# Optimization experiments

Hardware: AMD Instinct MI355X
Metric: run time of the kernel (lower is better)

Reference implementation:

```python
import jax, jax.numpy as jnp
import numpy as np

B, N, F, H, MH = 8, 1024, 768, 12, 3072
DH = F // H
EPS = 1e-5

def _ln(x, g, b):
    mu = jnp.mean(x, axis=-1, keepdims=True)
    var = jnp.mean(jnp.square(x - mu), axis=-1, keepdims=True)
    return (x - mu) * jax.lax.rsqrt(var + EPS) * g + b

def setup_inputs() -> dict:
    key = jax.random.key(0)
    ks = jax.random.split(key, 16)
    s = 1.0 / np.sqrt(F)
    sm = 1.0 / np.sqrt(MH)
    return {
        "x": jax.random.normal(ks[0], (B, N, F), dtype=jnp.float32),
        "Wq": jax.random.uniform(ks[1], (F, F), jnp.float32, -s, s),
        "bq": jax.random.uniform(ks[2], (F,), jnp.float32, -s, s),
        "Wk": jax.random.uniform(ks[3], (F, F), jnp.float32, -s, s),
        "bk": jax.random.uniform(ks[4], (F,), jnp.float32, -s, s),
        "Wv": jax.random.uniform(ks[5], (F, F), jnp.float32, -s, s),
        "bv": jax.random.uniform(ks[6], (F,), jnp.float32, -s, s),
        "Wo": jax.random.uniform(ks[7], (F, F), jnp.float32, -s, s),
        "bo": jax.random.uniform(ks[8], (F,), jnp.float32, -s, s),
        "ln1_g": jnp.ones((F,), jnp.float32),
        "ln1_b": jnp.zeros((F,), jnp.float32),
        "ln2_g": jnp.ones((F,), jnp.float32),
        "ln2_b": jnp.zeros((F,), jnp.float32),
        "W1": jax.random.uniform(ks[9], (F, MH), jnp.float32, -s, s),
        "b1": jax.random.uniform(ks[10], (MH,), jnp.float32, -s, s),
        "W2": jax.random.uniform(ks[11], (MH, F), jnp.float32, -sm, sm),
        "b2": jax.random.uniform(ks[12], (F,), jnp.float32, -sm, sm),
    }

def reference(x, Wq, bq, Wk, bk, Wv, bv, Wo, bo, ln1_g, ln1_b, ln2_g, ln2_b, W1, b1, W2, b2):
    xn = _ln(x, ln1_g, ln1_b)
    # low-rank (here full-rank, rank=-1) QKV projections, split into heads -> [b,h,n,dh]
    q = (xn @ Wq + bq).reshape(B, N, H, DH).transpose(0, 2, 1, 3)
    k = (xn @ Wk + bk).reshape(B, N, H, DH).transpose(0, 2, 1, 3)
    v = (xn @ Wv + bv).reshape(B, N, H, DH).transpose(0, 2, 1, 3)
    # note: original scales by sqrt(feats), NOT sqrt(d_head)
    score = jax.nn.softmax(jnp.einsum('bhif,bhjf->bhij', q, k) / jnp.sqrt(jnp.float32(F)), axis=-1)
    attn = jnp.einsum('bhij,bhjf->bhif', score, v)
    attn = attn.transpose(0, 2, 1, 3).reshape(B, N, F)
    out = (attn @ Wo + bo) + x  # dropout p=0.0
    h = _ln(out, ln2_g, ln2_b)
    h = jax.nn.gelu(h @ W1 + b1, approximate=False)
    h = jax.nn.gelu(h @ W2 + b2, approximate=False)  # second GELU per source
    return h + out
```

## Files before the change

kernel.cpp:

```cpp
#include <hip/hip_runtime.h>
#include <math.h>

#define B_ 8
#define N_ 1024
#define F_ 768
#define H_ 12
#define DH_ 64
#define MH_ 3072
#define MROWS (B_ * N_)

typedef unsigned short u16;
typedef unsigned int u32;
typedef __bf16 bf16x8 __attribute__((ext_vector_type(8)));
typedef float f32x4 __attribute__((ext_vector_type(4)));

__device__ inline f32x4 mfma16(bf16x8 a, bf16x8 b, f32x4 c) {
  return __builtin_amdgcn_mfma_f32_16x16x32_bf16(a, b, c, 0, 0, 0);
}

__device__ inline u16 f2bu(float f) {
  u32 b = __builtin_bit_cast(u32, f);
  b += 0x7fffu + ((b >> 16) & 1u);
  return (u16)(b >> 16);
}
__device__ inline float bu2f(u16 u) {
  u32 x = ((u32)u) << 16;
  return __builtin_bit_cast(float, x);
}
__device__ inline float gelu_exact(float x) {
  return 0.5f * x * (1.0f + erff(x * 0.70710678118654752f));
}

#define AS1 __attribute__((address_space(1)))
#define AS3 __attribute__((address_space(3)))
__device__ inline void glds16(const void* g, void* l) {
  __builtin_amdgcn_global_load_lds((const AS1 void*)g, (AS3 void*)l, 16, 0, 0);
}

__device__ inline float ldf(const float* p) { return *p; }
__device__ inline float ldf(const u16* p) { return bu2f(*p); }

template <typename Tin>
__global__ __launch_bounds__(256) void transpose_bf16(
    const Tin* __restrict__ in, u16* __restrict__ out, int R, int C) {
  __shared__ float tile[64][65];
  size_t ibase = (size_t)blockIdx.z * (size_t)R * (size_t)C;
  size_t obase = (size_t)blockIdx.z * (size_t)R * (size_t)C;
  int r0 = blockIdx.y << 6, c0 = blockIdx.x << 6;
  int t = threadIdx.x;
#pragma unroll
  for (int i = 0; i < 16; ++i) {
    int idx = t + (i << 8);
    int r = idx >> 6, c = idx & 63;
    tile[r][c] = ldf(&in[ibase + (size_t)(r0 + r) * C + (c0 + c)]);
  }
  __syncthreads();
#pragma unroll
  for (int i = 0; i < 16; ++i) {
    int idx = t + (i << 8);
    int rr = idx >> 6, cc = idx & 63;
    out[obase + (size_t)(c0 + rr) * R + (r0 + cc)] = f2bu(tile[cc][rr]);
  }
}

__global__ __launch_bounds__(256) void concat_bias(
    const float* __restrict__ a, const float* __restrict__ b,
    const float* __restrict__ c, float* __restrict__ o) {
  int i = blockIdx.x * 256 + threadIdx.x;
  if (i < 768) o[i] = a[i];
  else if (i < 1536) o[i] = b[i - 768];
  else o[i] = c[i - 1536];
}

__global__ __launch_bounds__(256) void ln_to_bf16(
    const float* __restrict__ X, const float* __restrict__ gw,
    const float* __restrict__ bw, u16* __restrict__ Y) {
  int row = blockIdx.x;
  int t = threadIdx.x;
  const float* xr = X + (size_t)row * F_;
  float v0 = xr[t], v1 = xr[t + 256], v2 = xr[t + 512];
  float s = v0 + v1 + v2;
  float ss = v0 * v0 + v1 * v1 + v2 * v2;
#pragma unroll
  for (int off = 1; off < 64; off <<= 1) {
    s += __shfl_xor(s, off, 64);
    ss += __shfl_xor(ss, off, 64);
  }
  __shared__ float red[8];
  int wid = t >> 6, lane = t & 63;
  if (lane == 0) { red[wid] = s; red[4 + wid] = ss; }
  __syncthreads();
  s = red[0] + red[1] + red[2] + red[3];
  ss = red[4] + red[5] + red[6] + red[7];
  float mu = s * (1.0f / F_);
  float var = ss * (1.0f / F_) - mu * mu;
  float rstd = rsqrtf(var + 1e-5f);
  u16* yr = Y + (size_t)row * F_;
  yr[t] = f2bu((v0 - mu) * rstd * gw[t] + bw[t]);
  yr[t + 256] = f2bu((v1 - mu) * rstd * gw[t + 256] + bw[t + 256]);
  yr[t + 512] = f2bu((v2 - mu) * rstd * gw[t + 512] + bw[t + 512]);
}

template <int MODE>
__global__ __launch_bounds__(256) void gemm_bt(
    const u16* __restrict__ A, const u16* __restrict__ Bt,
    const float* __restrict__ bias, void* __restrict__ outp,
    const float* __restrict__ resid, int Ndim, int Kdim, float qscale) {
  __shared__ __attribute__((aligned(16))) u16 As[2][128][32];
  __shared__ __attribute__((aligned(16))) u16 Bs[2][128][32];
  int t = threadIdx.x;
  int lane = t & 63, wid = t >> 6;

  int nwg = gridDim.x;
  int q8 = nwg >> 3;
  int bid = blockIdx.x;
  int swz = (bid & 7) * q8 + (bid >> 3);
  int nnt = Ndim >> 7;
  int mt = swz / nnt, nt = swz - mt * nnt;
  int row0 = mt << 7, col0 = nt << 7;

  int wr = (wid >> 1) << 6, wc = (wid & 1) << 6;
  int lr = lane & 15, lk = (lane >> 4) << 3;
  int rbase = (lane >> 4) << 2;
  f32x4 zero = {0.f, 0.f, 0.f, 0.f};
  f32x4 acc[4][4];
#pragma unroll
  for (int m = 0; m < 4; ++m)
#pragma unroll
    for (int n = 0; n < 4; ++n) acc[m][n] = zero;

  int o0 = (wid << 10) + (lane << 4);
  int srow = o0 >> 6;
  int scol = (o0 & 63) >> 1;
  const u16* Ag = A + (size_t)(row0 + srow) * Kdim + scol;
  const u16* Bg = Bt + (size_t)(col0 + srow) * Kdim + scol;
  char* AsB = (char*)&As[0][0][0] + (wid << 10);
  char* BsB = (char*)&Bs[0][0][0] + (wid << 10);
  size_t half = (size_t)64 * Kdim;

  auto STAGE = [&](int buf, int kt) {
    int bo = buf << 13;
    glds16(Ag + kt, AsB + bo);
    glds16(Ag + kt + half, AsB + bo + 4096);
    glds16(Bg + kt, BsB + bo);
    glds16(Bg + kt + half, BsB + bo + 4096);
  };

  STAGE(0, 0);
  __syncthreads();
  int nk = Kdim >> 5;
  for (int ki = 0; ki < nk; ++ki) {
    int buf = ki & 1;
    if (ki + 1 < nk) STAGE(buf ^ 1, (ki + 1) << 5);
    bf16x8 af[4], bfr[4];
#pragma unroll
    for (int m = 0; m < 4; ++m) af[m] = *(const bf16x8*)&As[buf][wr + (m << 4) + lr][lk];
#pragma unroll
    for (int n = 0; n < 4; ++n) bfr[n] = *(const bf16x8*)&Bs[buf][wc + (n << 4) + lr][lk];
#pragma unroll
    for (int m = 0; m < 4; ++m)
#pragma unroll
      for (int n = 0; n < 4; ++n) acc[m][n] = mfma16(af[m], bfr[n], acc[m][n]);
    __syncthreads();
  }

#pragma unroll
  for (int n = 0; n < 4; ++n) {
    int col = col0 + wc + (n << 4) + lr;
    float bc = bias[col];
    int sub = 0, hh = 0, dh = 0;
    float sc = 1.0f;
    if constexpr (MODE == 0) {
      sub = (col >= 1536) ? 2 : (col >= 768 ? 1 : 0);
      int c = col - sub * 768;
      hh = c >> 6; dh = c & 63;
      sc = (sub == 0) ? qscale : 1.0f;
    }
#pragma unroll
    for (int m = 0; m < 4; ++m) {
#pragma unroll
      for (int r = 0; r < 4; ++r) {
        int row = row0 + wr + (m << 4) + rbase + r;
        float val = acc[m][n][r] + bc;
        if constexpr (MODE == 0) {
          int b = row >> 10, nn = row & 1023;
          ((u16*)outp)[(size_t)sub * 6291456 +
                       ((((size_t)b * H_ + hh) << 10) + nn) * DH_ + dh] = f2bu(val * sc);
        } else if constexpr (MODE == 1) {
          val += resid[(size_t)row * Ndim + col];
          ((float*)outp)[(size_t)row * Ndim + col] = val;
        } else if constexpr (MODE == 2) {
          ((u16*)outp)[(size_t)row * Ndim + col] = f2bu(gelu_exact(val));
        } else {
          val = gelu_exact(val) + resid[(size_t)row * Ndim + col];
          ((float*)outp)[(size_t)row * Ndim + col] = val;
        }
      }
    }
  }
}

__global__ __launch_bounds__(256, 3) void attn_fwd(
    const u16* __restrict__ Q, const u16* __restrict__ K,
    const u16* __restrict__ Vt, u16* __restrict__ Aout) {
  __shared__ __attribute__((aligned(16))) u16 Ks[64][72];
  __shared__ __attribute__((aligned(16))) u16 Vs[64][72];
  __shared__ __attribute__((aligned(16))) u16 Ps[4][32][72];
  int t = threadIdx.x, lane = t & 63, wid = t >> 6;

  int bid = blockIdx.x;
  int swz = (bid & 7) * 96 + (bid >> 3);
  int bh = swz >> 3;
  int qt = swz & 7;
  int q0 = (qt << 7) + (wid << 5);

  int lr = lane & 15, lk = (lane >> 4) << 3;
  int rbase = (lane >> 4) << 2;

  bf16x8 qf[2][2];
#pragma unroll
  for (int m = 0; m < 2; ++m)
#pragma unroll
    for (int ks = 0; ks < 2; ++ks)
      qf[m][ks] = *(const bf16x8*)&Q[((size_t)bh * N_ + q0 + (m << 4) + lr) * DH_ + (ks << 5) + lk];

  float lsum[2][4];
  f32x4 zero = {0.f, 0.f, 0.f, 0.f};
  f32x4 Oacc[2][4];
#pragma unroll
  for (int m = 0; m < 2; ++m) {
#pragma unroll
    for (int r = 0; r < 4; ++r) lsum[m][r] = 0.f;
#pragma unroll
    for (int nd = 0; nd < 4; ++nd) Oacc[m][nd] = zero;
  }

  int srow = t >> 3;
  int scol = (t & 7) << 3;
  const u16* Kg = K + ((size_t)bh * N_ + srow) * DH_ + scol;
  const u16* Vg = Vt + ((size_t)bh * DH_ + srow) * N_ + scol;

  for (int kt = 0; kt < 16; ++kt) {
    __syncthreads();
    *(uint4*)&Ks[srow][scol]      = *(const uint4*)(Kg + (size_t)(kt << 6) * DH_);
    *(uint4*)&Ks[srow + 32][scol] = *(const uint4*)(Kg + (size_t)((kt << 6) + 32) * DH_);
    *(uint4*)&Vs[srow][scol]      = *(const uint4*)(Vg + (kt << 6));
    *(uint4*)&Vs[srow + 32][scol] = *(const uint4*)(Vg + (size_t)32 * N_ + (kt << 6));
    __syncthreads();

    f32x4 s[2][4];
#pragma unroll
    for (int m = 0; m < 2; ++m)
#pragma unroll
      for (int n = 0; n < 4; ++n) s[m][n] = zero;
#pragma unroll
    for (int ks = 0; ks < 2; ++ks) {
      bf16x8 kf[4];
#pragma unroll
      for (int n = 0; n < 4; ++n) kf[n] = *(const bf16x8*)&Ks[(n << 4) + lr][(ks << 5) + lk];
#pragma unroll
      for (int m = 0; m < 2; ++m)
#pragma unroll
        for (int n = 0; n < 4; ++n) s[m][n] = mfma16(qf[m][ks], kf[n], s[m][n]);
    }

#pragma unroll
    for (int m = 0; m < 2; ++m)
#pragma unroll
      for (int n = 0; n < 4; ++n)
#pragma unroll
        for (int r = 0; r < 4; ++r) {
          float p = exp2f(s[m][n][r]);
          lsum[m][r] += p;
          Ps[wid][(m << 4) + rbase + r][(n << 4) + lr] = f2bu(p);
        }

#pragma unroll
    for (int ks = 0; ks < 2; ++ks) {
      bf16x8 pf[2], vf[4];
#pragma unroll
      for (int m = 0; m < 2; ++m) pf[m] = *(const bf16x8*)&Ps[wid][(m << 4) + lr][(ks << 5) + lk];
#pragma unroll
      for (int nd = 0; nd < 4; ++nd) vf[nd] = *(const bf16x8*)&Vs[(nd << 4) + lr][(ks << 5) + lk];
#pragma unroll
      for (int m = 0; m < 2; ++m)
#pragma unroll
        for (int nd = 0; nd < 4; ++nd) Oacc[m][nd] = mfma16(pf[m], vf[nd], Oacc[m][nd]);
    }
  }

  int b = bh / H_, h = bh % H_;
#pragma unroll
  for (int m = 0; m < 2; ++m)
#pragma unroll
    for (int r = 0; r < 4; ++r) {
      float sv = lsum[m][r];
#pragma unroll
      for (int off = 1; off < 16; off <<= 1) sv += __shfl_xor(sv, off, 64);
      float inv = 1.0f / sv;
      int row = q0 + (m << 4) + rbase + r;
      size_t orow = ((size_t)b * N_ + row) * F_ + (size_t)h * DH_;
#pragma unroll
      for (int nd = 0; nd < 4; ++nd)
        Aout[orow + (nd << 4) + lr] = f2bu(Oacc[m][nd][r] * inv);
    }
}

extern "C" void kernel_launch(void* const* d_in, const int* in_sizes, int n_in,
                              void* d_out, int out_size, void* d_ws, size_t ws_size,
                              hipStream_t stream) {
  (void)in_sizes; (void)n_in; (void)out_size; (void)ws_size;
  const float* x   = (const float*)d_in[0];
  const float* Wq  = (const float*)d_in[1];
  const float* bq  = (const float*)d_in[2];
  const float* Wk  = (const float*)d_in[3];
  const float* bk  = (const float*)d_in[4];
  const float* Wv  = (const float*)d_in[5];
  const float* bv  = (const float*)d_in[6];
  const float* Wo  = (const float*)d_in[7];
  const float* bo  = (const float*)d_in[8];
  const float* g1  = (const float*)d_in[9];
  const float* bn1 = (const float*)d_in[10];
  const float* g2  = (const float*)d_in[11];
  const float* bn2 = (const float*)d_in[12];
  const float* W1  = (const float*)d_in[13];
  const float* b1  = (const float*)d_in[14];
  const float* W2  = (const float*)d_in[15];
  const float* b2  = (const float*)d_in[16];

  char* ws = (char*)d_ws;
  size_t off = 0;
  auto alloc = [&](size_t bytes) {
    char* p = ws + off;
    off += (bytes + 255) & ~(size_t)255;
    return p;
  };
  u16* Wqkvt = (u16*)alloc((size_t)3 * F_ * F_ * 2);
  u16* Wot  = (u16*)alloc((size_t)F_ * F_ * 2);
  u16* W1t  = (u16*)alloc((size_t)MH_ * F_ * 2);
  u16* W2t  = (u16*)alloc((size_t)MH_ * F_ * 2);
  float* bqkv = (float*)alloc((size_t)3 * F_ * 4);
  u16* xn  = (u16*)alloc((size_t)MROWS * F_ * 2);
  u16* qb  = (u16*)alloc((size_t)B_ * H_ * N_ * DH_ * 2);
  u16* kb  = (u16*)alloc((size_t)B_ * H_ * N_ * DH_ * 2);
  u16* vb  = (u16*)alloc((size_t)B_ * H_ * N_ * DH_ * 2);
  u16* vt  = (u16*)alloc((size_t)B_ * H_ * N_ * DH_ * 2);
  u16* attn = (u16*)alloc((size_t)MROWS * F_ * 2);
  float* outb = (float*)alloc((size_t)MROWS * F_ * 4);
  u16* h1 = qb;
  u16* hn = xn;

  const float QSCALE = 0.052058773227f;

  dim3 blk(256);
  transpose_bf16<float><<<dim3(12, 12, 1), blk, 0, stream>>>(Wq, Wqkvt, F_, F_);
  transpose_bf16<float><<<dim3(12, 12, 1), blk, 0, stream>>>(Wk, Wqkvt + (size_t)F_ * F_, F_, F_);
  transpose_bf16<float><<<dim3(12, 12, 1), blk, 0, stream>>>(Wv, Wqkvt + (size_t)2 * F_ * F_, F_, F_);
  transpose_bf16<float><<<dim3(12, 12, 1), blk, 0, stream>>>(Wo, Wot, F_, F_);
  transpose_bf16<float><<<dim3(48, 12, 1), blk, 0, stream>>>(W1, W1t, F_, MH_);
  transpose_bf16<float><<<dim3(12, 48, 1), blk, 0, stream>>>(W2, W2t, MH_, F_);
  concat_bias<<<dim3(9), blk, 0, stream>>>(bq, bk, bv, bqkv);
  ln_to_bf16<<<dim3(MROWS), blk, 0, stream>>>(x, g1, bn1, xn);
  gemm_bt<0><<<dim3(18 * 64), blk, 0, stream>>>(xn, Wqkvt, bqkv, qb, nullptr, 3 * F_, F_, QSCALE);
  transpose_bf16<u16><<<dim3(1, 16, 96), blk, 0, stream>>>(vb, vt, N_, DH_);
  attn_fwd<<<dim3(768), blk, 0, stream>>>(qb, kb, vt, attn);
  gemm_bt<1><<<dim3(6 * 64), blk, 0, stream>>>(attn, Wot, bo, outb, x, F_, F_, 1.0f);
  ln_to_bf16<<<dim3(MROWS), blk, 0, stream>>>(outb, g2, bn2, hn);
  gemm_bt<2><<<dim3(24 * 64), blk, 0, stream>>>(hn, W1t, b1, h1, nullptr, MH_, F_, 1.0f);
  gemm_bt<3><<<dim3(6 * 64), blk, 0, stream>>>(h1, W2t, b2, d_out, outb, F_, MH_, 1.0f);
}
```

Baseline: 318.7 us.

## Shrink GEMM tiles to 128x64, merge weight prep kernels, prefetch attention KV

```diff
diff --git a/kernel.cpp b/kernel.cpp
--- a/kernel.cpp
+++ b/kernel.cpp
@@ -37,39 +37,58 @@
   __builtin_amdgcn_global_load_lds((const AS1 void*)g, (AS3 void*)l, 16, 0, 0);
 }
 
-__device__ inline float ldf(const float* p) { return *p; }
-__device__ inline float ldf(const u16* p) { return bu2f(*p); }
-
-template <typename Tin>
-__global__ __launch_bounds__(256) void transpose_bf16(
-    const Tin* __restrict__ in, u16* __restrict__ out, int R, int C) {
+__global__ __launch_bounds__(256) void prep_weights(
+    const float* __restrict__ Wq, const float* __restrict__ Wk,
+    const float* __restrict__ Wv, const float* __restrict__ Wo,
+    const float* __restrict__ W1, const float* __restrict__ W2,
+    u16* __restrict__ Wqkvt, u16* __restrict__ Wot,
+    u16* __restrict__ W1t, u16* __restrict__ W2t) {
   __shared__ float tile[64][65];
-  size_t ibase = (size_t)blockIdx.z * (size_t)R * (size_t)C;
-  size_t obase = (size_t)blockIdx.z * (size_t)R * (size_t)C;
+  int z = blockIdx.z;
+  const float* in; u16* out; int R, C;
+  if (z == 0)      { in = Wq; out = Wqkvt;                       R = 768;  C = 768; }
+  else if (z == 1) { in = Wk; out = Wqkvt + 768 * 768;           R = 768;  C = 768; }
+  else if (z == 2) { in = Wv; out = Wqkvt + 2 * 768 * 768;       R = 768;  C = 768; }
+  else if (z == 3) { in = Wo; out = Wot;                         R = 768;  C = 768; }
+  else if (z == 4) { in = W1; out = W1t;                         R = 768;  C = 3072; }
+  else             { in = W2; out = W2t;                         R = 3072; C = 768; }
   int r0 = blockIdx.y << 6, c0 = blockIdx.x << 6;
+  if (r0 >= R || c0 >= C) return;
   int t = threadIdx.x;
 #pragma unroll
   for (int i = 0; i < 16; ++i) {
     int idx = t + (i << 8);
     int r = idx >> 6, c = idx & 63;
-    tile[r][c] = ldf(&in[ibase + (size_t)(r0 + r) * C + (c0 + c)]);
+    tile[r][c] = in[(size_t)(r0 + r) * C + (c0 + c)];
   }
   __syncthreads();
 #pragma unroll
   for (int i = 0; i < 16; ++i) {
     int idx = t + (i << 8);
     int rr = idx >> 6, cc = idx & 63;
-    out[obase + (size_t)(c0 + rr) * R + (r0 + cc)] = f2bu(tile[cc][rr]);
-  }
-}
-
-__global__ __launch_bounds__(256) void concat_bias(
-    const float* __restrict__ a, const float* __restrict__ b,
-    const float* __restrict__ c, float* __restrict__ o) {
-  int i = blockIdx.x * 256 + threadIdx.x;
-  if (i < 768) o[i] = a[i];
-  else if (i < 1536) o[i] = b[i - 768];
-  else o[i] = c[i - 1536];
+    out[(size_t)(c0 + rr) * R + (r0 + cc)] = f2bu(tile[cc][rr]);
+  }
+}
+
+__global__ __launch_bounds__(256) void transpose_v(
+    const u16* __restrict__ in, u16* __restrict__ out, int R, int C) {
+  __shared__ float tile[64][65];
+  size_t base = (size_t)blockIdx.z * (size_t)R * (size_t)C;
+  int r0 = blockIdx.y << 6, c0 = blockIdx.x << 6;
+  int t = threadIdx.x;
+#pragma unroll
+  for (int i = 0; i < 16; ++i) {
+    int idx = t + (i << 8);
+    int r = idx >> 6, c = idx & 63;
+    tile[r][c] = bu2f(in[base + (size_t)(r0 + r) * C + (c0 + c)]);
+  }
+  __syncthreads();
+#pragma unroll
+  for (int i = 0; i < 16; ++i) {
+    int idx = t + (i << 8);
+    int rr = idx >> 6, cc = idx & 63;
+    out[base + (size_t)(c0 + rr) * R + (r0 + cc)] = f2bu(tile[cc][rr]);
+  }
 }
 
 __global__ __launch_bounds__(256) void ln_to_bf16(
@@ -102,12 +121,13 @@
 }
 
 template <int MODE>
-__global__ __launch_bounds__(256) void gemm_bt(
+__global__ __launch_bounds__(256, 4) void gemm_t(
     const u16* __restrict__ A, const u16* __restrict__ Bt,
-    const float* __restrict__ bias, void* __restrict__ outp,
+    const float* __restrict__ b0, const float* __restrict__ b1,
+    const float* __restrict__ b2, void* __restrict__ outp,
     const float* __restrict__ resid, int Ndim, int Kdim, float qscale) {
   __shared__ __attribute__((aligned(16))) u16 As[2][128][32];
-  __shared__ __attribute__((aligned(16))) u16 Bs[2][128][32];
+  __shared__ __attribute__((aligned(16))) u16 Bs[2][64][32];
   int t = threadIdx.x;
   int lane = t & 63, wid = t >> 6;
 
@@ -115,23 +135,23 @@
   int q8 = nwg >> 3;
   int bid = blockIdx.x;
   int swz = (bid & 7) * q8 + (bid >> 3);
-  int nnt = Ndim >> 7;
+  int nnt = Ndim >> 6;
   int mt = swz / nnt, nt = swz - mt * nnt;
-  int row0 = mt << 7, col0 = nt << 7;
-
-  int wr = (wid >> 1) << 6, wc = (wid & 1) << 6;
+  int row0 = mt << 7, col0 = nt << 6;
+
+  int wr = (wid >> 1) << 6;
+  int wc = (wid & 1) << 5;
   int lr = lane & 15, lk = (lane >> 4) << 3;
   int rbase = (lane >> 4) << 2;
   f32x4 zero = {0.f, 0.f, 0.f, 0.f};
-  f32x4 acc[4][4];
+  f32x4 acc[4][2];
 #pragma unroll
   for (int m = 0; m < 4; ++m)
 #pragma unroll
-    for (int n = 0; n < 4; ++n) acc[m][n] = zero;
-
-  int o0 = (wid << 10) + (lane << 4);
-  int srow = o0 >> 6;
-  int scol = (o0 & 63) >> 1;
+    for (int n = 0; n < 2; ++n) acc[m][n] = zero;
+
+  int srow = (wid << 4) + (lane >> 2);
+  int scol = (lane & 3) << 3;
   const u16* Ag = A + (size_t)(row0 + srow) * Kdim + scol;
   const u16* Bg = Bt + (size_t)(col0 + srow) * Kdim + scol;
   char* AsB = (char*)&As[0][0][0] + (wid << 10);
@@ -139,11 +159,9 @@
   size_t half = (size_t)64 * Kdim;
 
   auto STAGE = [&](int buf, int kt) {
-    int bo = buf << 13;
-    glds16(Ag + kt, AsB + bo);
-    glds16(Ag + kt + half, AsB + bo + 4096);
-    glds16(Bg + kt, BsB + bo);
-    glds16(Bg + kt + half, BsB + bo + 4096);
+    glds16(Ag + kt, AsB + (buf << 13));
+    glds16(Ag + kt + half, AsB + (buf << 13) + 4096);
+    glds16(Bg + kt, BsB + (buf << 12));
   };
 
   STAGE(0, 0);
@@ -152,29 +170,32 @@
   for (int ki = 0; ki < nk; ++ki) {
     int buf = ki & 1;
     if (ki + 1 < nk) STAGE(buf ^ 1, (ki + 1) << 5);
-    bf16x8 af[4], bfr[4];
+    bf16x8 af[4], bfr[2];
 #pragma unroll
     for (int m = 0; m < 4; ++m) af[m] = *(const bf16x8*)&As[buf][wr + (m << 4) + lr][lk];
 #pragma unroll
-    for (int n = 0; n < 4; ++n) bfr[n] = *(const bf16x8*)&Bs[buf][wc + (n << 4) + lr][lk];
+    for (int n = 0; n < 2; ++n) bfr[n] = *(const bf16x8*)&Bs[buf][wc + (n << 4) + lr][lk];
 #pragma unroll
     for (int m = 0; m < 4; ++m)
 #pragma unroll
-      for (int n = 0; n < 4; ++n) acc[m][n] = mfma16(af[m], bfr[n], acc[m][n]);
+      for (int n = 0; n < 2; ++n) acc[m][n] = mfma16(af[m], bfr[n], acc[m][n]);
     __syncthreads();
   }
 
 #pragma unroll
-  for (int n = 0; n < 4; ++n) {
+  for (int n = 0; n < 2; ++n) {
     int col = col0 + wc + (n << 4) + lr;
-    float bc = bias[col];
+    float bc;
     int sub = 0, hh = 0, dh = 0;
     float sc = 1.0f;
     if constexpr (MODE == 0) {
       sub = (col >= 1536) ? 2 : (col >= 768 ? 1 : 0);
       int c = col - sub * 768;
+      bc = (sub == 0) ? b0[c] : (sub == 1 ? b1[c] : b2[c]);
       hh = c >> 6; dh = c & 63;
       sc = (sub == 0) ? qscale : 1.0f;
+    } else {
+      bc = b0[col];
     }
 #pragma unroll
     for (int m = 0; m < 4; ++m) {
@@ -183,9 +204,9 @@
         int row = row0 + wr + (m << 4) + rbase + r;
         float val = acc[m][n][r] + bc;
         if constexpr (MODE == 0) {
-          int b = row >> 10, nn = row & 1023;
+          int bb = row >> 10, nn = row & 1023;
           ((u16*)outp)[(size_t)sub * 6291456 +
-                       ((((size_t)b * H_ + hh) << 10) + nn) * DH_ + dh] = f2bu(val * sc);
+                       ((((size_t)bb * H_ + hh) << 10) + nn) * DH_ + dh] = f2bu(val * sc);
         } else if constexpr (MODE == 1) {
           val += resid[(size_t)row * Ndim + col];
           ((float*)outp)[(size_t)row * Ndim + col] = val;
@@ -240,12 +261,22 @@
   const u16* Kg = K + ((size_t)bh * N_ + srow) * DH_ + scol;
   const u16* Vg = Vt + ((size_t)bh * DH_ + srow) * N_ + scol;
 
+  uint4 kr0, kr1, vr0, vr1;
+  auto LOADKV = [&](int kt) {
+    kr0 = *(const uint4*)(Kg + (size_t)(kt << 6) * DH_);
+    kr1 = *(const uint4*)(Kg + (size_t)((kt << 6) + 32) * DH_);
+    vr0 = *(const uint4*)(Vg + (kt << 6));
+    vr1 = *(const uint4*)(Vg + (size_t)32 * N_ + (kt << 6));
+  };
+  LOADKV(0);
+
   for (int kt = 0; kt < 16; ++kt) {
     __syncthreads();
-    *(uint4*)&Ks[srow][scol]      = *(const uint4*)(Kg + (size_t)(kt << 6) * DH_);
-    *(uint4*)&Ks[srow + 32][scol] = *(const uint4*)(Kg + (size_t)((kt << 6) + 32) * DH_);
-    *(uint4*)&Vs[srow][scol]      = *(const uint4*)(Vg + (kt << 6));
-    *(uint4*)&Vs[srow + 32][scol] = *(const uint4*)(Vg + (size_t)32 * N_ + (kt << 6));
+    *(uint4*)&Ks[srow][scol]      = kr0;
+    *(uint4*)&Ks[srow + 32][scol] = kr1;
+    *(uint4*)&Vs[srow][scol]      = vr0;
+    *(uint4*)&Vs[srow + 32][scol] = vr1;
+    if (kt + 1 < 16) LOADKV(kt + 1);
     __syncthreads();
 
     f32x4 s[2][4];
@@ -339,7 +370,6 @@
   u16* Wot  = (u16*)alloc((size_t)F_ * F_ * 2);
   u16* W1t  = (u16*)alloc((size_t)MH_ * F_ * 2);
   u16* W2t  = (u16*)alloc((size_t)MH_ * F_ * 2);
-  float* bqkv = (float*)alloc((size_t)3 * F_ * 4);
   u16* xn  = (u16*)alloc((size_t)MROWS * F_ * 2);
   u16* qb  = (u16*)alloc((size_t)B_ * H_ * N_ * DH_ * 2);
   u16* kb  = (u16*)alloc((size_t)B_ * H_ * N_ * DH_ * 2);
@@ -353,19 +383,18 @@
   const float QSCALE = 0.052058773227f;
 
   dim3 blk(256);
-  transpose_bf16<float><<<dim3(12, 12, 1), blk, 0, stream>>>(Wq, Wqkvt, F_, F_);
-  transpose_bf16<float><<<dim3(12, 12, 1), blk, 0, stream>>>(Wk, Wqkvt + (size_t)F_ * F_, F_, F_);
-  transpose_bf16<float><<<dim3(12, 12, 1), blk, 0, stream>>>(Wv, Wqkvt + (size_t)2 * F_ * F_, F_, F_);
-  transpose_bf16<float><<<dim3(12, 12, 1), blk, 0, stream>>>(Wo, Wot, F_, F_);
-  transpose_bf16<float><<<dim3(48, 12, 1), blk, 0, stream>>>(W1, W1t, F_, MH_);
-  transpose_bf16<float><<<dim3(12, 48, 1), blk, 0, stream>>>(W2, W2t, MH_, F_);
-  concat_bias<<<dim3(9), blk, 0, stream>>>(bq, bk, bv, bqkv);
+  prep_weights<<<dim3(48, 48, 6), blk, 0, stream>>>(Wq, Wk, Wv, Wo, W1, W2,
+                                                    Wqkvt, Wot, W1t, W2t);
   ln_to_bf16<<<dim3(MROWS), blk, 0, stream>>>(x, g1, bn1, xn);
-  gemm_bt<0><<<dim3(18 * 64), blk, 0, stream>>>(xn, Wqkvt, bqkv, qb, nullptr, 3 * F_, F_, QSCALE);
-  transpose_bf16<u16><<<dim3(1, 16, 96), blk, 0, stream>>>(vb, vt, N_, DH_);
+  gemm_t<0><<<dim3(64 * 36), blk, 0, stream>>>(xn, Wqkvt, bq, bk, bv, qb,
+                                               nullptr, 3 * F_, F_, QSCALE);
+  transpose_v<<<dim3(1, 16, 96), blk, 0, stream>>>(vb, vt, N_, DH_);
   attn_fwd<<<dim3(768), blk, 0, stream>>>(qb, kb, vt, attn);
-  gemm_bt<1><<<dim3(6 * 64), blk, 0, stream>>>(attn, Wot, bo, outb, x, F_, F_, 1.0f);
+  gemm_t<1><<<dim3(64 * 12), blk, 0, stream>>>(attn, Wot, bo, nullptr, nullptr,
+                                               outb, x, F_, F_, 1.0f);
   ln_to_bf16<<<dim3(MROWS), blk, 0, stream>>>(outb, g2, bn2, hn);
-  gemm_bt<2><<<dim3(24 * 64), blk, 0, stream>>>(hn, W1t, b1, h1, nullptr, MH_, F_, 1.0f);
-  gemm_bt<3><<<dim3(6 * 64), blk, 0, stream>>>(h1, W2t, b2, d_out, outb, F_, MH_, 1.0f);
-}
+  gemm_t<2><<<dim3(64 * 48), blk, 0, stream>>>(hn, W1t, b1, nullptr, nullptr,
+                                               h1, nullptr, MH_, F_, 1.0f);
+  gemm_t<3><<<dim3(64 * 12), blk, 0, stream>>>(h1, W2t, b2, nullptr, nullptr,
+                                               d_out, outb, F_, MH_, 1.0f);
+}
```

Measured after the change: 317.7 us. About the same (-0.3%).
